# Performance work log

Measured on AMD Instinct MI355X. Metric: run time of the kernel, lower is better.

The kernel has to match this reference:

```python
import jax, jax.numpy as jnp
import numpy as np

H = 8          # num_heads
CHUNK = 68     # tokens_per_chunk = blocks_per_chunk(4) * tokens_per_block(17)
EPS = 1e-5


def _layer_norm(t, w, b):
    m = t.mean(-1, keepdims=True)
    v = t.var(-1, keepdims=True)
    return (t - m) / jnp.sqrt(v + EPS) * w + b


def _forward(tokens, embedding, Wq, bq, Wk, bk, Wv, bv, Wg, bg, Wo, bo,
             gn_w, gn_b, ln1_w, ln1_b, ln2_w, ln2_b, w1, b1, w2, b2):
    B, S = tokens.shape
    L, D, _ = Wq.shape
    dh = D // H
    n_chunks = S // CHUNK

    x = embedding[tokens]  # [B,S,D]

    # per-head decay gammas (standard RetNet)
    gamma = 1.0 - 2.0 ** (-5.0 - jnp.arange(H, dtype=jnp.float32))  # [H]

    # rotary relative-position tables (absolute positions, fresh state n=0)
    pos = jnp.arange(S, dtype=jnp.float32)
    inv = 1.0 / (10000.0 ** (jnp.arange(0, dh, 2, dtype=jnp.float32) / dh))
    ang = pos[:, None] * inv[None, :]                      # [S, dh/2]
    cs = jnp.concatenate([jnp.cos(ang)] * 2, -1)[None, :, None, :]  # [1,S,1,dh]
    sn = jnp.concatenate([jnp.sin(ang)] * 2, -1)[None, :, None, :]

    def rot(t):  # t: [B,S,H,dh]
        t1, t2 = jnp.split(t, 2, axis=-1)
        return t * cs + jnp.concatenate([-t2, t1], -1) * sn

    # chunkwise decay structures
    idx = jnp.arange(CHUNK, dtype=jnp.float32)
    expo = idx[:, None] - idx[None, :]
    Dmask = jnp.where(expo >= 0, gamma[:, None, None] ** expo[None], 0.0)  # [H,C,C]
    cross_dec = gamma[None, :] ** (idx[:, None] + 1.0)          # [C,H]
    k_dec = gamma[None, :] ** (CHUNK - 1.0 - idx[:, None])      # [C,H]
    chunk_dec = gamma ** CHUNK                                  # [H]

    for l in range(L):
        h = _layer_norm(x, ln1_w[l], ln1_b[l])
        q = rot((h @ Wq[l] + bq[l]).reshape(B, S, H, dh))
        k = rot((h @ Wk[l] + bk[l]).reshape(B, S, H, dh)) * (dh ** -0.5)
        v = (h @ Wv[l] + bv[l]).reshape(B, S, H, dh)
        # split into chunks, scan carries the per-head KV state [B,H,dh,dh]
        qc = q.reshape(B, n_chunks, CHUNK, H, dh).transpose(1, 0, 2, 3, 4)
        kc = k.reshape(B, n_chunks, CHUNK, H, dh).transpose(1, 0, 2, 3, 4)
        vc = v.reshape(B, n_chunks, CHUNK, H, dh).transpose(1, 0, 2, 3, 4)

        def step(state, qkv):
            qq, kk, vv = qkv  # each [B,C,H,dh]
            inner = jnp.einsum('bihd,bjhd->bhij', qq, kk) * Dmask
            out = jnp.einsum('bhij,bjhd->bihd', inner, vv)
            out = out + jnp.einsum('bihd,bhde->bihe', qq, state) * cross_dec[None, :, :, None]
            state = state * chunk_dec[None, :, None, None] + \
                jnp.einsum('bjhd,bjhe->bhde', kk * k_dec[None, :, :, None], vv)
            return state, out

        state0 = jnp.zeros((B, H, dh, dh), dtype=x.dtype)
        _, ret = jax.lax.scan(step, state0, (qc, kc, vc))
        ret = ret.transpose(1, 0, 2, 3, 4).reshape(B, S, H, dh)
        # per-head group norm
        m = ret.mean(-1, keepdims=True)
        vr = ret.var(-1, keepdims=True)
        ret = (ret - m) / jnp.sqrt(vr + EPS)
        ret = (ret * gn_w[l].reshape(H, dh) + gn_b[l].reshape(H, dh)).reshape(B, S, D)
        g = jax.nn.silu(h @ Wg[l] + bg[l])
        x = x + (g * ret) @ Wo[l] + bo[l]
        h2 = _layer_norm(x, ln2_w[l], ln2_b[l])
        x = x + jax.nn.silu(h2 @ w1[l] + b1[l]) @ w2[l] + b2[l]
    return x


def setup_inputs() -> dict:
    key = jax.random.key(0)
    B, S, D, L, FF, V = 16, 408, 512, 10, 2048, 519
    ks = jax.random.split(key, 16)
    r = lambda i, shape, s=0.02: jax.random.normal(ks[i], shape, dtype=jnp.float32) * s
    return {
        'tokens': jax.random.randint(ks[0], (B, S), 0, V, dtype=jnp.int32),
        'embedding': r(1, (V, D)),
        'Wq': r(2, (L, D, D)), 'bq': jnp.zeros((L, D), jnp.float32),
        'Wk': r(3, (L, D, D)), 'bk': jnp.zeros((L, D), jnp.float32),
        'Wv': r(4, (L, D, D)), 'bv': jnp.zeros((L, D), jnp.float32),
        'Wg': r(5, (L, D, D)), 'bg': jnp.zeros((L, D), jnp.float32),
        'Wo': r(6, (L, D, D)), 'bo': jnp.zeros((L, D), jnp.float32),
        'gn_w': jnp.ones((L, D), jnp.float32), 'gn_b': jnp.zeros((L, D), jnp.float32),
        'ln1_w': jnp.ones((L, D), jnp.float32), 'ln1_b': jnp.zeros((L, D), jnp.float32),
        'ln2_w': jnp.ones((L, D), jnp.float32), 'ln2_b': jnp.zeros((L, D), jnp.float32),
        'w1': r(7, (L, D, FF)), 'b1': jnp.zeros((L, FF), jnp.float32),
        'w2': r(8, (L, FF, D)), 'b2': jnp.zeros((L, D), jnp.float32),
    }


def reference(tokens, embedding, Wq, bq, Wk, bk, Wv, bv, Wg, bg, Wo, bo,
              gn_w, gn_b, ln1_w, ln1_b, ln2_w, ln2_b, w1, b1, w2, b2):
    return _forward(tokens, embedding, Wq, bq, Wk, bk, Wv, bv, Wg, bg, Wo, bo,
                    gn_w, gn_b, ln1_w, ln1_b, ln2_w, ln2_b, w1, b1, w2, b2)
```

## Files before the change

kernel.cpp:

```cpp
#include <hip/hip_runtime.h>
#include <hip/hip_bf16.h>

#define H 8
#define DH 64
#define DMODEL 512
#define SEQ 408
#define BATCH 16
#define NLAYER 10
#define FFDIM 2048
#define CHUNK 68
#define NCHUNK 6
#define M (BATCH*SEQ)
#define EPS 1e-5f

typedef __hip_bfloat16 bf16;
typedef unsigned short ushort_t;
typedef short bf8v __attribute__((ext_vector_type(8)));
typedef float f4v  __attribute__((ext_vector_type(4)));

static constexpr size_t QKVG_STRIDE = 2u*512*512;
static constexpr size_t QKVG_HL     = 512*512;
static constexpr size_t WO_HI = 0;
static constexpr size_t WO_LO = WO_HI + 512*512;
static constexpr size_t W1_HI = WO_LO + 512*512;
static constexpr size_t W1_LO = W1_HI + 2048*512;
static constexpr size_t W2_HI = W1_LO + 2048*512;
static constexpr size_t W2_LO = W2_HI + 512*2048;

__device__ __forceinline__ float us2f(unsigned short u){ return __uint_as_float(((unsigned)u) << 16); }
__device__ __forceinline__ unsigned short f2bfs(float f){
  __bf16 h = (__bf16)f;
  return *(unsigned short*)&h;
}
__device__ __forceinline__ void split2(float f, unsigned short& hi, unsigned short& lo){
  hi = f2bfs(f);
  lo = f2bfs(f - us2f(hi));
}

typedef const __attribute__((address_space(1))) unsigned int* gas_ptr;
typedef __attribute__((address_space(3))) unsigned int* las_ptr;
__device__ __forceinline__ void gld16(const void* g, void* l){
  __builtin_amdgcn_global_load_lds((gas_ptr)g, (las_ptr)l, 16, 0, 0);
}

__device__ __forceinline__ int xcd_swz(int fid, int nwg){
  int q = nwg >> 3;
  return (fid & 7) * q + (fid >> 3);
}

__global__ void embed_kernel(const int* __restrict__ tokens, const float* __restrict__ emb,
                             float* __restrict__ x){
  int idx = blockIdx.x*256 + threadIdx.x;
  if (idx >= M*DMODEL) return;
  int r = idx >> 9; int d = idx & 511;
  x[idx] = emb[(size_t)tokens[r]*DMODEL + d];
}

__global__ void rope_table_kernel(float* __restrict__ tab){
  int idx = blockIdx.x*256 + threadIdx.x;
  if (idx >= SEQ*32) return;
  int s = idx >> 5, i = idx & 31;
  float inv = powf(10000.0f, -(float)(2*i) * (1.0f/64.0f));
  float ang = (float)s * inv;
  float sn, c; sincosf(ang, &sn, &c);
  tab[idx] = c;
  tab[SEQ*32 + idx] = sn;
}

__global__ __launch_bounds__(256) void ln_kernel(const float* __restrict__ x,
    const float* __restrict__ w, const float* __restrict__ b,
    ushort_t* __restrict__ hhi, ushort_t* __restrict__ hlo){
  __shared__ float red[8];
  int r = blockIdx.x, tid = threadIdx.x;
  size_t base = (size_t)r*DMODEL;
  float v0 = x[base + tid], v1 = x[base + tid + 256];
  float s = v0 + v1, s2 = v0*v0 + v1*v1;
  int lane = tid & 63, wv = tid >> 6;
  #pragma unroll
  for (int o = 32; o; o >>= 1){ s += __shfl_xor(s, o); s2 += __shfl_xor(s2, o); }
  if (lane == 0){ red[wv] = s; red[wv+4] = s2; }
  __syncthreads();
  float tot  = red[0]+red[1]+red[2]+red[3];
  float tot2 = red[4]+red[5]+red[6]+red[7];
  float mean = tot * (1.0f/512.0f);
  float var  = tot2 * (1.0f/512.0f) - mean*mean;
  float rinv = rsqrtf(var + EPS);
  float o0 = (v0-mean)*rinv*w[tid]     + b[tid];
  float o1 = (v1-mean)*rinv*w[tid+256] + b[tid+256];
  unsigned short hi, lo;
  split2(o0, hi, lo); hhi[base+tid] = hi; hlo[base+tid] = lo;
  split2(o1, hi, lo); hhi[base+tid+256] = hi; hlo[base+tid+256] = lo;
}

__device__ __forceinline__ void wsplit_tile(const float* __restrict__ W,
    ushort_t* __restrict__ hi, ushort_t* __restrict__ lo,
    int N, int K, int n0, int k0)
{
  __shared__ float tb[32][33];
  int tx = threadIdx.x & 31, ty = threadIdx.x >> 5;
  #pragma unroll
  for (int r = 0; r < 32; r += 8)
    tb[ty+r][tx] = W[(size_t)(k0+ty+r)*N + n0 + tx];
  __syncthreads();
  #pragma unroll
  for (int r = 0; r < 32; r += 8){
    float v = tb[tx][ty+r];
    unsigned short h, l; split2(v, h, l);
    size_t o = (size_t)(n0+ty+r)*K + k0 + tx;
    hi[o] = h; lo[o] = l;
  }
}

__global__ __launch_bounds__(256) void wsplit_qkvg_kernel(
    const float* __restrict__ Wq, const float* __restrict__ Wk,
    const float* __restrict__ Wv, const float* __restrict__ Wg,
    ushort_t* __restrict__ wsp)
{
  int z = blockIdx.z;
  const float* W = (z==0)?Wq:(z==1)?Wk:(z==2)?Wv:Wg;
  ushort_t* hi = wsp + (size_t)z*QKVG_STRIDE;
  wsplit_tile(W, hi, hi + QKVG_HL, 512, 512, blockIdx.x*32, blockIdx.y*32);
}

__global__ __launch_bounds__(256) void wsplit_ffo_kernel(
    const float* __restrict__ Wo, const float* __restrict__ w1,
    const float* __restrict__ w2, ushort_t* __restrict__ wsp)
{
  int b = blockIdx.x;
  const float* W; ushort_t* hi; int N, K, n0, k0;
  if (b < 256){
    W = Wo; hi = wsp + WO_HI; N = 512; K = 512;
    n0 = (b & 15)*32; k0 = (b >> 4)*32;
  } else if (b < 1280){
    int bb = b - 256;
    W = w1; hi = wsp + W1_HI; N = 2048; K = 512;
    n0 = (bb & 63)*32; k0 = (bb >> 6)*32;
  } else {
    int bb = b - 1280;
    W = w2; hi = wsp + W2_HI; N = 512; K = 2048;
    n0 = (bb & 15)*32; k0 = (bb >> 4)*32;
  }
  wsplit_tile(W, hi, hi + (size_t)N*K, N, K, n0, k0);
}

#define BK 32

template<int TBN>
__global__ __launch_bounds__(256) void gemm_ps_kernel(
    const ushort_t* __restrict__ Ahi, const ushort_t* __restrict__ Alo,
    const ushort_t* __restrict__ Bhi, const ushort_t* __restrict__ Blo,
    const float* __restrict__ bias,
    const float* Cin, float* Cout, ushort_t* Co_hi, ushort_t* Co_lo,
    int N, int K, int epi)
{
  constexpr int TNW = TBN/32;
  __shared__ __align__(16) short AsH[2][64*BK];
  __shared__ __align__(16) short AsL[2][64*BK];
  __shared__ __align__(16) short BsH[2][TBN*BK];
  __shared__ __align__(16) short BsL[2][TBN*BK];
  int tid = threadIdx.x;
  int lane = tid & 63, wave = tid >> 6;
  int wm = (wave >> 1) * 32, wn = (wave & 1) * (TBN/2);
  int l15 = lane & 15, quad = lane >> 4;

  int nwg = gridDim.x * gridDim.y;
  int fid = blockIdx.y * gridDim.x + blockIdx.x;
  int swz = xcd_swz(fid, nwg);
  int bn = (swz % gridDim.x) * TBN;
  int bm = (swz / gridDim.x) * 64;
  int Kloc = K / gridDim.z;
  int k0 = blockIdx.z * Kloc;

  f4v acc[2][TNW];
  #pragma unroll
  for (int i = 0; i < 2; i++)
    #pragma unroll
    for (int j = 0; j < TNW; j++) acc[i][j] = (f4v){0.f,0.f,0.f,0.f};

  int arow = tid >> 2, ak = (tid & 3) * 8;
  const ushort_t* aHp  = Ahi + (size_t)(bm + arow)*K + k0 + ak;
  const ushort_t* aLp  = Alo + (size_t)(bm + arow)*K + k0 + ak;
  const ushort_t* bHp  = Bhi + (size_t)(bn + arow)*K + k0 + ak;
  const ushort_t* bLp  = Blo + (size_t)(bn + arow)*K + k0 + ak;
  const ushort_t* bHp2 = Bhi + (size_t)(bn + 64 + arow)*K + k0 + ak;
  const ushort_t* bLp2 = Blo + (size_t)(bn + 64 + arow)*K + k0 + ak;

  auto STAGE = [&](int buf, int kofs){
    gld16(aHp + kofs, &AsH[buf][tid*8]);
    gld16(aLp + kofs, &AsL[buf][tid*8]);
    gld16(bHp + kofs, &BsH[buf][tid*8]);
    gld16(bLp + kofs, &BsL[buf][tid*8]);
    if constexpr (TBN == 128){
      gld16(bHp2 + kofs, &BsH[buf][tid*8 + 2048]);
      gld16(bLp2 + kofs, &BsL[buf][tid*8 + 2048]);
    }
  };

  STAGE(0, 0);
  STAGE(1, BK);
  const int nt = Kloc / BK;
  for (int t = 0; t < nt; t++){
    if (t + 1 < nt){
      if constexpr (TBN == 128) asm volatile("s_waitcnt vmcnt(6)" ::: "memory");
      else                      asm volatile("s_waitcnt vmcnt(4)" ::: "memory");
    } else {
      asm volatile("s_waitcnt vmcnt(0)" ::: "memory");
    }
    __builtin_amdgcn_s_barrier();
    asm volatile("" ::: "memory");
    int cur = t & 1;
    bf8v afh[2], afl[2], bfh[TNW], bfl[TNW];
    #pragma unroll
    for (int i = 0; i < 2; i++){
      afh[i] = *(const bf8v*)&AsH[cur][(wm + i*16 + l15)*BK + quad*8];
      afl[i] = *(const bf8v*)&AsL[cur][(wm + i*16 + l15)*BK + quad*8];
    }
    #pragma unroll
    for (int j = 0; j < TNW; j++){
      bfh[j] = *(const bf8v*)&BsH[cur][(wn + j*16 + l15)*BK + quad*8];
      bfl[j] = *(const bf8v*)&BsL[cur][(wn + j*16 + l15)*BK + quad*8];
    }
    #pragma unroll
    for (int i = 0; i < 2; i++)
      #pragma unroll
      for (int j = 0; j < TNW; j++){
        acc[i][j] = __builtin_amdgcn_mfma_f32_16x16x32_bf16(afh[i], bfl[j], acc[i][j], 0, 0, 0);
        acc[i][j] = __builtin_amdgcn_mfma_f32_16x16x32_bf16(afl[i], bfh[j], acc[i][j], 0, 0, 0);
        acc[i][j] = __builtin_amdgcn_mfma_f32_16x16x32_bf16(afh[i], bfh[j], acc[i][j], 0, 0, 0);
      }
    asm volatile("s_waitcnt lgkmcnt(0)" ::: "memory");
    __builtin_amdgcn_s_barrier();
    asm volatile("" ::: "memory");
    if (t + 2 < nt) STAGE(cur, (t+2)*BK);
  }
  #pragma unroll
  for (int i = 0; i < 2; i++){
    int m0 = bm + wm + i*16 + quad*4;
    #pragma unroll
    for (int j = 0; j < TNW; j++){
      int n = bn + wn + j*16 + l15;
      float bsv = bias[n];
      #pragma unroll
      for (int r = 0; r < 4; r++){
        int m = m0 + r;
        if (epi == 3){
          float c = acc[i][j][r] + (blockIdx.z == 0 ? bsv : 0.0f);
          atomicAdd(&Cout[(size_t)m*N + n], c);
          continue;
        }
        float c = acc[i][j][r] + bsv;
        if (epi == 1) c = c / (1.0f + expf(-c));
        if (epi == 2) c += Cin[(size_t)m*N + n];
        if (Co_hi){
          unsigned short hi, lo; split2(c, hi, lo);
          Co_hi[(size_t)m*N + n] = hi;
          Co_lo[(size_t)m*N + n] = lo;
        } else {
          Cout[(size_t)m*N + n] = c;
        }
      }
    }
  }
}

__global__ __launch_bounds__(256) void gemm_qkvg_kernel(
    const ushort_t* __restrict__ Ahi, const ushort_t* __restrict__ Alo,
    const ushort_t* __restrict__ wsp,
    const float* __restrict__ bq, const float* __restrict__ bk,
    const float* __restrict__ bv, const float* __restrict__ bg,
    float* __restrict__ qo, float* __restrict__ ko,
    float* __restrict__ vo, float* __restrict__ go)
{
  const int N = DMODEL, K = DMODEL;
  __shared__ __align__(16) short AsH[2][64*BK];
  __shared__ __align__(16) short AsL[2][64*BK];
  __shared__ __align__(16) short BsH[2][64*BK];
  __shared__ __align__(16) short BsL[2][64*BK];
  int tid = threadIdx.x;
  int lane = tid & 63, wave = tid >> 6;
  int wm = (wave >> 1) * 32, wn = (wave & 1) * 32;
  int l15 = lane & 15, quad = lane >> 4;

  int nwg = gridDim.x * gridDim.y;
  int fid = blockIdx.y * gridDim.x + blockIdx.x;
  int swz = xcd_swz(fid, nwg);
  int bx = swz % gridDim.x;
  int which = bx >> 3;
  int bn = (bx & 7) * 64;
  int bm = (swz / gridDim.x) * 64;

  const ushort_t* Bhi = wsp + (size_t)which * QKVG_STRIDE;
  const ushort_t* Blo = Bhi + QKVG_HL;
  const float* bias = (which==0) ? bq : (which==1) ? bk : (which==2) ? bv : bg;
  float* out        = (which==0) ? qo : (which==1) ? ko : (which==2) ? vo : go;

  f4v acc[2][2];
  #pragma unroll
  for (int i = 0; i < 2; i++)
    #pragma unroll
    for (int j = 0; j < 2; j++) acc[i][j] = (f4v){0.f,0.f,0.f,0.f};

  int arow = tid >> 2, ak = (tid & 3) * 8;
  const ushort_t* aHp = Ahi + (size_t)(bm + arow)*K + ak;
  const ushort_t* aLp = Alo + (size_t)(bm + arow)*K + ak;
  const ushort_t* bHp = Bhi + (size_t)(bn + arow)*K + ak;
  const ushort_t* bLp = Blo + (size_t)(bn + arow)*K + ak;

  auto STAGE = [&](int buf, int kofs){
    gld16(aHp + kofs, &AsH[buf][tid*8]);
    gld16(aLp + kofs, &AsL[buf][tid*8]);
    gld16(bHp + kofs, &BsH[buf][tid*8]);
    gld16(bLp + kofs, &BsL[buf][tid*8]);
  };

  STAGE(0, 0);
  STAGE(1, BK);
  const int nt = K / BK;
  for (int t = 0; t < nt; t++){
    if (t + 1 < nt) asm volatile("s_waitcnt vmcnt(4)" ::: "memory");
    else            asm volatile("s_waitcnt vmcnt(0)" ::: "memory");
    __builtin_amdgcn_s_barrier();
    asm volatile("" ::: "memory");
    int cur = t & 1;
    bf8v afh[2], afl[2], bfh[2], bfl[2];
    #pragma unroll
    for (int i = 0; i < 2; i++){
      afh[i] = *(const bf8v*)&AsH[cur][(wm + i*16 + l15)*BK + quad*8];
      afl[i] = *(const bf8v*)&AsL[cur][(wm + i*16 + l15)*BK + quad*8];
      bfh[i] = *(const bf8v*)&BsH[cur][(wn + i*16 + l15)*BK + quad*8];
      bfl[i] = *(const bf8v*)&BsL[cur][(wn + i*16 + l15)*BK + quad*8];
    }
    #pragma unroll
    for (int i = 0; i < 2; i++)
      #pragma unroll
      for (int j = 0; j < 2; j++){
        acc[i][j] = __builtin_amdgcn_mfma_f32_16x16x32_bf16(afh[i], bfl[j], acc[i][j], 0, 0, 0);
        acc[i][j] = __builtin_amdgcn_mfma_f32_16x16x32_bf16(afl[i], bfh[j], acc[i][j], 0, 0, 0);
        acc[i][j] = __builtin_amdgcn_mfma_f32_16x16x32_bf16(afh[i], bfh[j], acc[i][j], 0, 0, 0);
      }
    asm volatile("s_waitcnt lgkmcnt(0)" ::: "memory");
    __builtin_amdgcn_s_barrier();
    asm volatile("" ::: "memory");
    if (t + 2 < nt) STAGE(cur, (t+2)*BK);
  }
  #pragma unroll
  for (int i = 0; i < 2; i++){
    int m0 = bm + wm + i*16 + quad*4;
    #pragma unroll
    for (int j = 0; j < 2; j++){
      int n = bn + wn + j*16 + l15;
      float bsv = bias[n];
      #pragma unroll
      for (int r = 0; r < 4; r++){
        int m = m0 + r;
        float c = acc[i][j][r] + bsv;
        if (which == 3) c = c / (1.0f + expf(-c));
        out[(size_t)m*N + n] = c;
      }
    }
  }
}

__global__ __launch_bounds__(256) void ret_chunkkv_kernel(
    const float* __restrict__ k, const float* __restrict__ v,
    const float* __restrict__ tab, float* __restrict__ Ast)
{
  __shared__ __align__(16) float kT[DH][CHUNK];
  __shared__ __align__(16) float vs[CHUNK][DH];
  __shared__ float gpw[CHUNK];
  int tid = threadIdx.x;
  int c = blockIdx.x % NCHUNK;
  int bh = blockIdx.x / NCHUNK;
  int hh = bh & 7, b = bh >> 3;
  float gamma = 1.0f - exp2f(-5.0f - (float)hh);
  if (tid < CHUNK) gpw[tid] = powf(gamma, (float)(CHUNK-1-tid));
  size_t rowbase = ((size_t)(b*SEQ + c*CHUNK))*DMODEL + hh*DH;
  for (int e = tid; e < CHUNK*DH; e += 256){
    int i = e >> 6, d = e & 63;
    size_t g  = rowbase + (size_t)i*DMODEL + d;
    size_t gp = rowbase + (size_t)i*DMODEL + (d ^ 32);
    int s = c*CHUNK + i, ii = d & 31;
    float cs = tab[s*32 + ii], sn = tab[SEQ*32 + s*32 + ii];
    float k1 = k[g], k2 = k[gp];
    float kr = (d < 32) ? (k1*cs - k2*sn) : (k1*cs + k2*sn);
    kT[d][i] = kr * 0.125f;
    vs[i][d] = v[g];
  }
  __syncthreads();
  float* A = Ast + (size_t)blockIdx.x * (DH*DH);
  for (int e = tid; e < DH*16; e += 256){
    int d = e >> 4, q4 = (e & 15) * 4;
    float4 a4 = {0,0,0,0};
    for (int j = 0; j < CHUNK; j++){
      float kj = kT[d][j] * gpw[j];
      float4 v4 = *(const float4*)&vs[j][q4];
      a4.x += kj*v4.x; a4.y += kj*v4.y; a4.z += kj*v4.z; a4.w += kj*v4.w;
    }
    *(float4*)&A[d*DH + q4] = a4;
  }
}

__global__ __launch_bounds__(256) void ret_scan_kernel(float* __restrict__ Ast)
{
  int bh = blockIdx.x, hh = bh & 7;
  float gamma = 1.0f - exp2f(-5.0f - (float)hh);
  float chdec = powf(gamma, (float)CHUNK);
  int tid = threadIdx.x;
  float4 run[4];
  #pragma unroll
  for (int t = 0; t < 4; t++) run[t] = (float4){0,0,0,0};
  size_t base = (size_t)bh * NCHUNK * (DH*DH) + (size_t)tid*16;
  for (int c = 0; c < NCHUNK; c++){
    float4* slot = (float4*)(Ast + base + (size_t)c*(DH*DH));
    float4 a[4];
    #pragma unroll
    for (int t = 0; t < 4; t++) a[t] = slot[t];
    #pragma unroll
    for (int t = 0; t < 4; t++) slot[t] = run[t];
    #pragma unroll
    for (int t = 0; t < 4; t++){
      run[t].x = run[t].x*chdec + a[t].x;
      run[t].y = run[t].y*chdec + a[t].y;
      run[t].z = run[t].z*chdec + a[t].z;
      run[t].w = run[t].w*chdec + a[t].w;
    }
  }
}

__global__ __launch_bounds__(256) void ret_out_kernel(
    const float* __restrict__ q, const float* __restrict__ k, const float* __restrict__ v,
    const float* __restrict__ tab, const float* __restrict__ Ast, float* __restrict__ ret)
{
  __shared__ __align__(16) float qs[CHUNK][DH];
  __shared__ __align__(16) float kT[DH][CHUNK];
  __shared__ __align__(16) float vs[CHUNK][DH];
  __shared__ __align__(16) float sts[DH*DH];
  __shared__ float inner[34][CHUNK];
  __shared__ float gpw[CHUNK];
  int tid = threadIdx.x;
  int c = blockIdx.x % NCHUNK;
  int bh = blockIdx.x / NCHUNK;
  int hh = bh & 7, b = bh >> 3;
  float gamma = 1.0f - exp2f(-5.0f - (float)hh);
  if (tid < CHUNK) gpw[tid] = powf(gamma, (float)tid);
  size_t rowbase = ((size_t)(b*SEQ + c*CHUNK))*DMODEL + hh*DH;
  for (int e = tid; e < CHUNK*DH; e += 256){
    int i = e >> 6, d = e & 63;
    size_t g  = rowbase + (size_t)i*DMODEL + d;
    size_t gp = rowbase + (size_t)i*DMODEL + (d ^ 32);
    int s = c*CHUNK + i, ii = d & 31;
    float cs = tab[s*32 + ii], sn = tab[SEQ*32 + s*32 + ii];
    float q1 = q[g], q2 = q[gp];
    float k1 = k[g], k2 = k[gp];
    if (d < 32){
      qs[i][d] = q1*cs - q2*sn;
      kT[d][i] = (k1*cs - k2*sn) * 0.125f;
    } else {
      qs[i][d] = q1*cs + q2*sn;
      kT[d][i] = (k1*cs + k2*sn) * 0.125f;
    }
    vs[i][d] = v[g];
  }
  const float* st = Ast + (size_t)blockIdx.x * (DH*DH);
  for (int e = tid*4; e < DH*DH; e += 1024)
    *(float4*)&sts[e] = *(const float4*)&st[e];
  __syncthreads();
  for (int p = 0; p < 2; p++){
    int i0 = p*34;
    for (int e = tid; e < 34*CHUNK; e += 256){
      int ii = e / CHUNK, j = e - ii*CHUNK;
      int i = i0 + ii;
      float val = 0.0f;
      if (j <= i){
        float dot = 0.0f;
        #pragma unroll 16
        for (int d = 0; d < DH; d++) dot += qs[i][d] * kT[d][j];
        val = dot * gpw[i-j];
      }
      inner[ii][j] = val;
    }
    __syncthreads();
    for (int e = tid; e < 34*16; e += 256){
      int ii = e >> 4, q4 = (e & 15) * 4;
      int i = i0 + ii;
      float4 o4 = {0,0,0,0};
      for (int j = 0; j <= i; j++){
        float w = inner[ii][j];
        float4 v4 = *(const float4*)&vs[j][q4];
        o4.x += w*v4.x; o4.y += w*v4.y; o4.z += w*v4.z; o4.w += w*v4.w;
      }
      float4 c4 = {0,0,0,0};
      #pragma unroll 8
      for (int e2 = 0; e2 < DH; e2++){
        float qv = qs[i][e2];
        float4 s4 = *(const float4*)&sts[e2*DH + q4];
        c4.x += qv*s4.x; c4.y += qv*s4.y; c4.z += qv*s4.z; c4.w += qv*s4.w;
      }
      float cd = gpw[i] * gamma;
      size_t ob = rowbase + (size_t)i*DMODEL + q4;
      float4 o; o.x = o4.x + cd*c4.x; o.y = o4.y + cd*c4.y;
      o.z = o4.z + cd*c4.z; o.w = o4.w + cd*c4.w;
      *(float4*)&ret[ob] = o;
    }
    __syncthreads();
  }
}

__global__ __launch_bounds__(512) void gnorm_gate_kernel(const float* __restrict__ ret,
    const float* __restrict__ g, const float* __restrict__ gnw, const float* __restrict__ gnb,
    ushort_t* __restrict__ ohi, ushort_t* __restrict__ olo)
{
  int r = blockIdx.x, tid = threadIdx.x;
  size_t idx = (size_t)r*DMODEL + tid;
  float val = ret[idx];
  float s = val, s2 = val*val;
  #pragma unroll
  for (int o = 32; o; o >>= 1){ s += __shfl_xor(s, o); s2 += __shfl_xor(s2, o); }
  float mean = s * (1.0f/64.0f);
  float var  = s2 * (1.0f/64.0f) - mean*mean;
  float y = (val - mean) * rsqrtf(var + EPS);
  y = y * gnw[tid] + gnb[tid];
  y = y * g[idx];
  unsigned short hi, lo; split2(y, hi, lo);
  ohi[idx] = hi; olo[idx] = lo;
}

__global__ void outwrite_kernel(const float* __restrict__ x, float* __restrict__ out){
  int idx = blockIdx.x*256 + threadIdx.x;
  if (idx < M*DMODEL) out[idx] = x[idx];
}

extern "C" void kernel_launch(void* const* d_in, const int* in_sizes, int n_in,
                              void* d_out, int out_size, void* d_ws, size_t ws_size,
                              hipStream_t stream)
{
  (void)in_sizes; (void)n_in; (void)out_size; (void)ws_size;
  const int*   tokens = (const int*)d_in[0];
  const float* emb  = (const float*)d_in[1];
  const float* Wq = (const float*)d_in[2];  const float* bq = (const float*)d_in[3];
  const float* Wk = (const float*)d_in[4];  const float* bk = (const float*)d_in[5];
  const float* Wv = (const float*)d_in[6];  const float* bv = (const float*)d_in[7];
  const float* Wg = (const float*)d_in[8];  const float* bg = (const float*)d_in[9];
  const float* Wo = (const float*)d_in[10]; const float* bo = (const float*)d_in[11];
  const float* gnw = (const float*)d_in[12]; const float* gnb = (const float*)d_in[13];
  const float* ln1w = (const float*)d_in[14]; const float* ln1b = (const float*)d_in[15];
  const float* ln2w = (const float*)d_in[16]; const float* ln2b = (const float*)d_in[17];
  const float* w1 = (const float*)d_in[18]; const float* b1 = (const float*)d_in[19];
  const float* w2 = (const float*)d_in[20]; const float* b2 = (const float*)d_in[21];

  const size_t MD = (size_t)M*DMODEL;
  float* xf = (float*)d_ws;
  float* qf = xf + MD;
  float* kf = qf + MD;
  float* vf = kf + MD;
  float* gf = vf + MD;
  float* rf = gf + MD;
  ushort_t* h_hi = (ushort_t*)(rf + MD);
  ushort_t* h_lo = h_hi + MD;
  float* Ast = (float*)h_hi;
  ushort_t* rg_hi = h_hi;
  ushort_t* rg_lo = h_lo;
  ushort_t* ff_hi = (ushort_t*)qf;
  ushort_t* ff_lo = (ushort_t*)vf;
  ushort_t* wsp = (ushort_t*)rf;
  float* ropetab = (float*)(h_lo + MD);

  embed_kernel<<<(M*DMODEL)/256, 256, 0, stream>>>(tokens, emb, xf);
  rope_table_kernel<<<(SEQ*32 + 255)/256, 256, 0, stream>>>(ropetab);

  dim3 gqkvg(32, M/64);
  dim3 g512(DMODEL/64, M/64);
  dim3 gff(FFDIM/64, M/64);
  dim3 gw2(DMODEL/64, M/64, 4);
  dim3 gsplit4(16, 16, 4);
  for (int l = 0; l < NLAYER; l++){
    const size_t wO = (size_t)l*DMODEL*DMODEL;
    const size_t bO = (size_t)l*DMODEL;
    const size_t w1O = (size_t)l*DMODEL*FFDIM;
    const size_t b1O = (size_t)l*FFDIM;
    wsplit_qkvg_kernel<<<gsplit4, 256, 0, stream>>>(Wq + wO, Wk + wO, Wv + wO, Wg + wO, wsp);
    ln_kernel<<<M, 256, 0, stream>>>(xf, ln1w + bO, ln1b + bO, h_hi, h_lo);
    gemm_qkvg_kernel<<<gqkvg, 256, 0, stream>>>(h_hi, h_lo, wsp,
        bq + bO, bk + bO, bv + bO, bg + bO,
        qf, kf, vf, gf);
    ret_chunkkv_kernel<<<BATCH*H*NCHUNK, 256, 0, stream>>>(kf, vf, ropetab, Ast);
    ret_scan_kernel<<<BATCH*H, 256, 0, stream>>>(Ast);
    ret_out_kernel<<<BATCH*H*NCHUNK, 256, 0, stream>>>(qf, kf, vf, ropetab, Ast, rf);
    gnorm_gate_kernel<<<M, 512, 0, stream>>>(rf, gf, gnw + bO, gnb + bO, rg_hi, rg_lo);
    wsplit_ffo_kernel<<<2304, 256, 0, stream>>>(Wo + wO, w1 + w1O, w2 + w1O, wsp);
    gemm_ps_kernel<64><<<g512, 256, 0, stream>>>(rg_hi, rg_lo,
        wsp + WO_HI, wsp + WO_LO, bo + bO, xf, xf, nullptr, nullptr, DMODEL, DMODEL, 2);
    ln_kernel<<<M, 256, 0, stream>>>(xf, ln2w + bO, ln2b + bO, h_hi, h_lo);
    gemm_ps_kernel<64><<<gff, 256, 0, stream>>>(h_hi, h_lo,
        wsp + W1_HI, wsp + W1_LO, b1 + b1O, nullptr, nullptr, ff_hi, ff_lo, FFDIM, DMODEL, 1);
    gemm_ps_kernel<64><<<gw2, 256, 0, stream>>>(ff_hi, ff_lo,
        wsp + W2_HI, wsp + W2_LO, b2 + bO, nullptr, xf, nullptr, nullptr, DMODEL, FFDIM, 3);
  }
  outwrite_kernel<<<(M*DMODEL)/256, 256, 0, stream>>>(xf, (float*)d_out);
}
```

Measured before the change: 3.776 ms.

## Fuse group-norm gating into retention output and weight split into layernorm

```diff
diff --git a/kernel.cpp b/kernel.cpp
--- a/kernel.cpp
+++ b/kernel.cpp
@@ -17,6 +17,7 @@
 typedef unsigned short ushort_t;
 typedef short bf8v __attribute__((ext_vector_type(8)));
 typedef float f4v  __attribute__((ext_vector_type(4)));
+typedef unsigned short us4 __attribute__((ext_vector_type(4)));
 
 static constexpr size_t QKVG_STRIDE = 2u*512*512;
 static constexpr size_t QKVG_HL     = 512*512;
@@ -67,11 +68,43 @@
   tab[SEQ*32 + idx] = sn;
 }
 
-__global__ __launch_bounds__(256) void ln_kernel(const float* __restrict__ x,
-    const float* __restrict__ w, const float* __restrict__ b,
-    ushort_t* __restrict__ hhi, ushort_t* __restrict__ hlo){
+__device__ __forceinline__ void wsplit_tile(const float* __restrict__ W,
+    ushort_t* __restrict__ hi, ushort_t* __restrict__ lo,
+    int N, int K, int n0, int k0)
+{
+  __shared__ float tb[32][33];
+  int tx = threadIdx.x & 31, ty = threadIdx.x >> 5;
+  #pragma unroll
+  for (int r = 0; r < 32; r += 8)
+    tb[ty+r][tx] = W[(size_t)(k0+ty+r)*N + n0 + tx];
+  __syncthreads();
+  #pragma unroll
+  for (int r = 0; r < 32; r += 8){
+    float v = tb[tx][ty+r];
+    unsigned short h, l; split2(v, h, l);
+    size_t o = (size_t)(n0+ty+r)*K + k0 + tx;
+    hi[o] = h; lo[o] = l;
+  }
+}
+
+__global__ __launch_bounds__(256) void ln_wsplit_kernel(
+    const float* __restrict__ x, const float* __restrict__ w, const float* __restrict__ b,
+    ushort_t* __restrict__ hhi, ushort_t* __restrict__ hlo,
+    const float* __restrict__ Wq, const float* __restrict__ Wk,
+    const float* __restrict__ Wv, const float* __restrict__ Wg,
+    ushort_t* __restrict__ wsp)
+{
+  int bid = blockIdx.x;
+  if (bid >= M){
+    int t = bid - M;
+    int z = t >> 8, tile = t & 255;
+    const float* W = (z==0)?Wq:(z==1)?Wk:(z==2)?Wv:Wg;
+    ushort_t* hi = wsp + (size_t)z*QKVG_STRIDE;
+    wsplit_tile(W, hi, hi + QKVG_HL, 512, 512, (tile & 15)*32, (tile >> 4)*32);
+    return;
+  }
   __shared__ float red[8];
-  int r = blockIdx.x, tid = threadIdx.x;
+  int r = bid, tid = threadIdx.x;
   size_t base = (size_t)r*DMODEL;
   float v0 = x[base + tid], v1 = x[base + tid + 256];
   float s = v0 + v1, s2 = v0*v0 + v1*v1;
@@ -92,34 +125,29 @@
   split2(o1, hi, lo); hhi[base+tid+256] = hi; hlo[base+tid+256] = lo;
 }
 
-__device__ __forceinline__ void wsplit_tile(const float* __restrict__ W,
-    ushort_t* __restrict__ hi, ushort_t* __restrict__ lo,
-    int N, int K, int n0, int k0)
-{
-  __shared__ float tb[32][33];
-  int tx = threadIdx.x & 31, ty = threadIdx.x >> 5;
-  #pragma unroll
-  for (int r = 0; r < 32; r += 8)
-    tb[ty+r][tx] = W[(size_t)(k0+ty+r)*N + n0 + tx];
+__global__ __launch_bounds__(256) void ln_kernel(const float* __restrict__ x,
+    const float* __restrict__ w, const float* __restrict__ b,
+    ushort_t* __restrict__ hhi, ushort_t* __restrict__ hlo){
+  __shared__ float red[8];
+  int r = blockIdx.x, tid = threadIdx.x;
+  size_t base = (size_t)r*DMODEL;
+  float v0 = x[base + tid], v1 = x[base + tid + 256];
+  float s = v0 + v1, s2 = v0*v0 + v1*v1;
+  int lane = tid & 63, wv = tid >> 6;
+  #pragma unroll
+  for (int o = 32; o; o >>= 1){ s += __shfl_xor(s, o); s2 += __shfl_xor(s2, o); }
+  if (lane == 0){ red[wv] = s; red[wv+4] = s2; }
   __syncthreads();
-  #pragma unroll
-  for (int r = 0; r < 32; r += 8){
-    float v = tb[tx][ty+r];
-    unsigned short h, l; split2(v, h, l);
-    size_t o = (size_t)(n0+ty+r)*K + k0 + tx;
-    hi[o] = h; lo[o] = l;
-  }
-}
-
-__global__ __launch_bounds__(256) void wsplit_qkvg_kernel(
-    const float* __restrict__ Wq, const float* __restrict__ Wk,
-    const float* __restrict__ Wv, const float* __restrict__ Wg,
-    ushort_t* __restrict__ wsp)
-{
-  int z = blockIdx.z;
-  const float* W = (z==0)?Wq:(z==1)?Wk:(z==2)?Wv:Wg;
-  ushort_t* hi = wsp + (size_t)z*QKVG_STRIDE;
-  wsplit_tile(W, hi, hi + QKVG_HL, 512, 512, blockIdx.x*32, blockIdx.y*32);
+  float tot  = red[0]+red[1]+red[2]+red[3];
+  float tot2 = red[4]+red[5]+red[6]+red[7];
+  float mean = tot * (1.0f/512.0f);
+  float var  = tot2 * (1.0f/512.0f) - mean*mean;
+  float rinv = rsqrtf(var + EPS);
+  float o0 = (v0-mean)*rinv*w[tid]     + b[tid];
+  float o1 = (v1-mean)*rinv*w[tid+256] + b[tid+256];
+  unsigned short hi, lo;
+  split2(o0, hi, lo); hhi[base+tid] = hi; hlo[base+tid] = lo;
+  split2(o1, hi, lo); hhi[base+tid+256] = hi; hlo[base+tid+256] = lo;
 }
 
 __global__ __launch_bounds__(256) void wsplit_ffo_kernel(
@@ -429,7 +457,9 @@
 
 __global__ __launch_bounds__(256) void ret_out_kernel(
     const float* __restrict__ q, const float* __restrict__ k, const float* __restrict__ v,
-    const float* __restrict__ tab, const float* __restrict__ Ast, float* __restrict__ ret)
+    const float* __restrict__ tab, const float* __restrict__ Ast,
+    const float* __restrict__ g, const float* __restrict__ gnw, const float* __restrict__ gnb,
+    ushort_t* __restrict__ rg_hi, ushort_t* __restrict__ rg_lo)
 {
   __shared__ __align__(16) float qs[CHUNK][DH];
   __shared__ __align__(16) float kT[DH][CHUNK];
@@ -446,12 +476,12 @@
   size_t rowbase = ((size_t)(b*SEQ + c*CHUNK))*DMODEL + hh*DH;
   for (int e = tid; e < CHUNK*DH; e += 256){
     int i = e >> 6, d = e & 63;
-    size_t g  = rowbase + (size_t)i*DMODEL + d;
+    size_t gg = rowbase + (size_t)i*DMODEL + d;
     size_t gp = rowbase + (size_t)i*DMODEL + (d ^ 32);
     int s = c*CHUNK + i, ii = d & 31;
     float cs = tab[s*32 + ii], sn = tab[SEQ*32 + s*32 + ii];
-    float q1 = q[g], q2 = q[gp];
-    float k1 = k[g], k2 = k[gp];
+    float q1 = q[gg], q2 = q[gp];
+    float k1 = k[gg], k2 = k[gp];
     if (d < 32){
       qs[i][d] = q1*cs - q2*sn;
       kT[d][i] = (k1*cs - k2*sn) * 0.125f;
@@ -459,7 +489,7 @@
       qs[i][d] = q1*cs + q2*sn;
       kT[d][i] = (k1*cs + k2*sn) * 0.125f;
     }
-    vs[i][d] = v[g];
+    vs[i][d] = v[gg];
   }
   const float* st = Ast + (size_t)blockIdx.x * (DH*DH);
   for (int e = tid*4; e < DH*DH; e += 1024)
@@ -497,32 +527,36 @@
         c4.x += qv*s4.x; c4.y += qv*s4.y; c4.z += qv*s4.z; c4.w += qv*s4.w;
       }
       float cd = gpw[i] * gamma;
-      size_t ob = rowbase + (size_t)i*DMODEL + q4;
       float4 o; o.x = o4.x + cd*c4.x; o.y = o4.y + cd*c4.y;
       o.z = o4.z + cd*c4.z; o.w = o4.w + cd*c4.w;
-      *(float4*)&ret[ob] = o;
+      float s = o.x + o.y + o.z + o.w;
+      float s2 = o.x*o.x + o.y*o.y + o.z*o.z + o.w*o.w;
+      #pragma unroll
+      for (int off = 1; off < 16; off <<= 1){
+        s  += __shfl_xor(s,  off);
+        s2 += __shfl_xor(s2, off);
+      }
+      float mean = s * (1.0f/64.0f);
+      float var  = s2 * (1.0f/64.0f) - mean*mean;
+      float rinv = rsqrtf(var + EPS);
+      size_t gb = rowbase + (size_t)i*DMODEL + q4;
+      float4 gv = *(const float4*)&g[gb];
+      int gn0 = hh*64 + q4;
+      float y0 = ((o.x-mean)*rinv*gnw[gn0+0] + gnb[gn0+0]) * gv.x;
+      float y1 = ((o.y-mean)*rinv*gnw[gn0+1] + gnb[gn0+1]) * gv.y;
+      float y2 = ((o.z-mean)*rinv*gnw[gn0+2] + gnb[gn0+2]) * gv.z;
+      float y3 = ((o.w-mean)*rinv*gnw[gn0+3] + gnb[gn0+3]) * gv.w;
+      us4 vh, vl;
+      unsigned short hi, lo;
+      split2(y0, hi, lo); vh[0] = hi; vl[0] = lo;
+      split2(y1, hi, lo); vh[1] = hi; vl[1] = lo;
+      split2(y2, hi, lo); vh[2] = hi; vl[2] = lo;
+      split2(y3, hi, lo); vh[3] = hi; vl[3] = lo;
+      *(us4*)&rg_hi[gb] = vh;
+      *(us4*)&rg_lo[gb] = vl;
     }
     __syncthreads();
   }
-}
-
-__global__ __launch_bounds__(512) void gnorm_gate_kernel(const float* __restrict__ ret,
-    const float* __restrict__ g, const float* __restrict__ gnw, const float* __restrict__ gnb,
-    ushort_t* __restrict__ ohi, ushort_t* __restrict__ olo)
-{
-  int r = blockIdx.x, tid = threadIdx.x;
-  size_t idx = (size_t)r*DMODEL + tid;
-  float val = ret[idx];
-  float s = val, s2 = val*val;
-  #pragma unroll
-  for (int o = 32; o; o >>= 1){ s += __shfl_xor(s, o); s2 += __shfl_xor(s2, o); }
-  float mean = s * (1.0f/64.0f);
-  float var  = s2 * (1.0f/64.0f) - mean*mean;
-  float y = (val - mean) * rsqrtf(var + EPS);
-  y = y * gnw[tid] + gnb[tid];
-  y = y * g[idx];
-  unsigned short hi, lo; split2(y, hi, lo);
-  ohi[idx] = hi; olo[idx] = lo;
 }
 
 __global__ void outwrite_kernel(const float* __restrict__ x, float* __restrict__ out){
@@ -557,7 +591,7 @@
   float* rf = gf + MD;
   ushort_t* h_hi = (ushort_t*)(rf + MD);
   ushort_t* h_lo = h_hi + MD;
-  float* Ast = (float*)h_hi;
+  float* Ast = rf;
   ushort_t* rg_hi = h_hi;
   ushort_t* rg_lo = h_lo;
   ushort_t* ff_hi = (ushort_t*)qf;
@@ -572,21 +606,20 @@
   dim3 g512(DMODEL/64, M/64);
   dim3 gff(FFDIM/64, M/64);
   dim3 gw2(DMODEL/64, M/64, 4);
-  dim3 gsplit4(16, 16, 4);
   for (int l = 0; l < NLAYER; l++){
     const size_t wO = (size_t)l*DMODEL*DMODEL;
     const size_t bO = (size_t)l*DMODEL;
     const size_t w1O = (size_t)l*DMODEL*FFDIM;
     const size_t b1O = (size_t)l*FFDIM;
-    wsplit_qkvg_kernel<<<gsplit4, 256, 0, stream>>>(Wq + wO, Wk + wO, Wv + wO, Wg + wO, wsp);
-    ln_kernel<<<M, 256, 0, stream>>>(xf, ln1w + bO, ln1b + bO, h_hi, h_lo);
+    ln_wsplit_kernel<<<M + 1024, 256, 0, stream>>>(xf, ln1w + bO, ln1b + bO,
+        h_hi, h_lo, Wq + wO, Wk + wO, Wv + wO, Wg + wO, wsp);
     gemm_qkvg_kernel<<<gqkvg, 256, 0, stream>>>(h_hi, h_lo, wsp,
         bq + bO, bk + bO, bv + bO, bg + bO,
         qf, kf, vf, gf);
     ret_chunkkv_kernel<<<BATCH*H*NCHUNK, 256, 0, stream>>>(kf, vf, ropetab, Ast);
     ret_scan_kernel<<<BATCH*H, 256, 0, stream>>>(Ast);
-    ret_out_kernel<<<BATCH*H*NCHUNK, 256, 0, stream>>>(qf, kf, vf, ropetab, Ast, rf);
-    gnorm_gate_kernel<<<M, 512, 0, stream>>>(rf, gf, gnw + bO, gnb + bO, rg_hi, rg_lo);
+    ret_out_kernel<<<BATCH*H*NCHUNK, 256, 0, stream>>>(qf, kf, vf, ropetab, Ast,
+        gf, gnw + bO, gnb + bO, rg_hi, rg_lo);
     wsplit_ffo_kernel<<<2304, 256, 0, stream>>>(Wo + wO, w1 + w1O, w2 + w1O, wsp);
     gemm_ps_kernel<64><<<g512, 256, 0, stream>>>(rg_hi, rg_lo,
         wsp + WO_HI, wsp + WO_LO, bo + bO, xf, xf, nullptr, nullptr, DMODEL, DMODEL, 2);
```

New measurement: 3.752 ms. Within noise of the previous version (-0.6%).
